# Performance work log

Measured on AMD Instinct MI355X. Metric: run time of the kernel, lower is better.

Reference implementation:

```python
import jax, jax.numpy as jnp
import numpy as np

N_OSC = 256
BATCH = 1024
DT = 0.1
STEPS = 10


def setup_inputs() -> dict:
    key = jax.random.key(0)
    k_theta, k_K, k_omega = jax.random.split(key, 3)
    theta_init = jax.random.normal(k_theta, (BATCH, N_OSC), dtype=jnp.float32)
    K0 = jax.random.normal(k_K, (N_OSC, N_OSC), dtype=jnp.float32) * 0.1
    K = (K0 + K0.T) / 2  # symmetric coupling matrix, as in torch init
    omega = jax.random.normal(k_omega, (N_OSC,), dtype=jnp.float32) * 0.1
    K_global = jnp.float32(0.5)
    return {"theta_init": theta_init, "K": K, "omega": omega, "K_global": K_global}


def reference(theta_init, K, omega, K_global):
    n = K.shape[0]

    def step(theta, _):
        # diff[b, i, j] = theta[b, j] - theta[b, i]
        diff = theta[..., None, :] - theta[..., :, None]
        coupling_sum = jnp.sum(K * jnp.sin(diff), axis=-1)  # (batch, n)
        dtheta = omega + (K_global / n) * coupling_sum
        theta_new = theta + DT * dtheta
        # wrap to (-pi, pi]
        theta_new = jnp.arctan2(jnp.sin(theta_new), jnp.cos(theta_new))
        return theta_new, None

    theta, _ = jax.lax.scan(step, theta_init, None, length=STEPS)
    cos_mean = jnp.cos(theta).mean(axis=-1)
    sin_mean = jnp.sin(theta).mean(axis=-1)
    coherence = jnp.sqrt(cos_mean ** 2 + sin_mean ** 2)
    return theta, coherence
```

## Files before the change

kernel.cpp:

```cpp
#include <hip/hip_runtime.h>
#include <math.h>


typedef __attribute__((ext_vector_type(4))) float f32x4;

constexpr int N       = 256;
constexpr int RB      = 16;
constexpr int STEPS   = 10;
constexpr int WAVES   = 8;
constexpr int THREADS = WAVES * 64;
constexpr float DT    = 0.1f;
constexpr float TWO_PI     = 6.28318530717958648f;
constexpr float INV_TWO_PI = 0.15915494309189535f;

__global__ __launch_bounds__(THREADS, 2)
void kuramoto_fp8(const float* __restrict__ theta0,
                  const float* __restrict__ Kmat,
                  const float* __restrict__ omega,
                  const float* __restrict__ kglob,
                  float* __restrict__ theta_out,
                  float* __restrict__ coh_out)
{
    __shared__ __align__(16) unsigned char SC[2][RB][512];
    __shared__ float redS[RB][WAVES], redC[RB][WAVES];

    const int tid  = threadIdx.x;
    const int wv   = tid >> 6;
    const int lane = tid & 63;
    const int q    = lane >> 4;
    const int l15  = lane & 15;
    const int b0   = blockIdx.x * RB;

    const float kgn = kglob[0] * (1.0f / 256.0f);

    long kf[2][8];
#pragma unroll
    for (int t = 0; t < 2; ++t) {
        const int i = 32 * wv + 16 * t + l15;
        const float* kr = Kmat + (size_t)i * N + 8 * q;
#pragma unroll
        for (int c = 0; c < 8; ++c) {
            float4 lo = *(const float4*)(kr + 32 * c);
            float4 hi = *(const float4*)(kr + 32 * c + 4);
            int w0 = __builtin_amdgcn_cvt_pk_fp8_f32(lo.x, lo.y, 0, false);
            w0     = __builtin_amdgcn_cvt_pk_fp8_f32(lo.z, lo.w, w0, true);
            int w1 = __builtin_amdgcn_cvt_pk_fp8_f32(hi.x, hi.y, 0, false);
            w1     = __builtin_amdgcn_cvt_pk_fp8_f32(hi.z, hi.w, w1, true);
            kf[t][c] = (long)(unsigned)w0 | ((long)w1 << 32);
        }
    }

    float thv[2][4], om[2][4];
#pragma unroll
    for (int t = 0; t < 2; ++t)
#pragma unroll
        for (int r = 0; r < 4; ++r) {
            const int i = 32 * wv + 16 * t + 4 * q + r;
            om[t][r]  = omega[i];
            thv[t][r] = theta0[(size_t)(b0 + l15) * N + i];
        }

    float sv[2][4], cv[2][4];

    for (int s = 0; s < STEPS; ++s) {
        const int buf = s & 1;
#pragma unroll
        for (int t = 0; t < 2; ++t) {
#pragma unroll
            for (int r = 0; r < 4; ++r)
                __sincosf(thv[t][r], &sv[t][r], &cv[t][r]);
            int spk = __builtin_amdgcn_cvt_pk_fp8_f32(sv[t][0], sv[t][1], 0, false);
            spk     = __builtin_amdgcn_cvt_pk_fp8_f32(sv[t][2], sv[t][3], spk, true);
            int cpk = __builtin_amdgcn_cvt_pk_fp8_f32(cv[t][0], cv[t][1], 0, false);
            cpk     = __builtin_amdgcn_cvt_pk_fp8_f32(cv[t][2], cv[t][3], cpk, true);
            const int g = 8 * wv + 4 * t + q;
            const int u = (g >> 1) ^ l15;
            int2 val; val.x = spk; val.y = cpk;
            *(int2*)&SC[buf][l15][16 * u + 8 * (g & 1)] = val;
        }
        __syncthreads();

        f32x4 aS[2], aC[2];
#pragma unroll
        for (int t = 0; t < 2; ++t) {
            aS[t] = (f32x4){0.f, 0.f, 0.f, 0.f};
            aC[t] = (f32x4){0.f, 0.f, 0.f, 0.f};
        }
#pragma unroll
        for (int c = 0; c < 8; ++c) {
            const int uu = (4 * c + q) ^ l15;
            int4 vvv = *(const int4*)&SC[buf][l15][16 * uu];
            long Bs = (long)(unsigned)vvv.x | ((long)vvv.z << 32);
            long Bc = (long)(unsigned)vvv.y | ((long)vvv.w << 32);
#pragma unroll
            for (int t = 0; t < 2; ++t) {
                aS[t] = __builtin_amdgcn_mfma_f32_16x16x32_fp8_fp8(kf[t][c], Bs, aS[t], 0, 0, 0);
                aC[t] = __builtin_amdgcn_mfma_f32_16x16x32_fp8_fp8(kf[t][c], Bc, aC[t], 0, 0, 0);
            }
        }

#pragma unroll
        for (int t = 0; t < 2; ++t)
#pragma unroll
            for (int r = 0; r < 4; ++r) {
                float coup = cv[t][r] * aS[t][r] - sv[t][r] * aC[t][r];
                thv[t][r] = fmaf(DT, fmaf(kgn, coup, om[t][r]), thv[t][r]);
            }
    }

    float ps = 0.f, pc = 0.f;
#pragma unroll
    for (int t = 0; t < 2; ++t)
#pragma unroll
        for (int r = 0; r < 4; ++r) {
            float th = thv[t][r];
            float s0, c0;
            __sincosf(th, &s0, &c0);
            float w = fmaf(-TWO_PI, rintf(th * INV_TWO_PI), th);
            theta_out[(size_t)(b0 + l15) * N + 32 * wv + 16 * t + 4 * q + r] = w;
            ps += s0; pc += c0;
        }
    ps += __shfl_xor(ps, 16, 64);  pc += __shfl_xor(pc, 16, 64);
    ps += __shfl_xor(ps, 32, 64);  pc += __shfl_xor(pc, 32, 64);
    if (q == 0) { redS[l15][wv] = ps; redC[l15][wv] = pc; }
    __syncthreads();
    if (tid < RB) {
        float S = 0.f, C = 0.f;
#pragma unroll
        for (int k = 0; k < WAVES; ++k) { S += redS[tid][k]; C += redC[tid][k]; }
        float sm = S * (1.0f / 256.0f);
        float cm = C * (1.0f / 256.0f);
        coh_out[b0 + tid] = sqrtf(sm * sm + cm * cm);
    }
}

extern "C" void kernel_launch(void* const* d_in, const int* in_sizes, int n_in,
                              void* d_out, int out_size, void* d_ws, size_t ws_size,
                              hipStream_t stream) {
    const float* theta0 = (const float*)d_in[0];
    const float* Kmat   = (const float*)d_in[1];
    const float* omega  = (const float*)d_in[2];
    const float* kglob  = (const float*)d_in[3];

    float* theta_out = (float*)d_out;
    float* coh_out   = theta_out + 1024 * N;

    kuramoto_fp8<<<dim3(1024 / RB), dim3(THREADS), 0, stream>>>(
        theta0, Kmat, omega, kglob, theta_out, coh_out);
}
```

Baseline: 75.19 us.

## Prepack K to fp8 in a separate kernel and update sin/cos via angle-addition polynomials

A small pre-kernel converts K to fp8 in MFMA fragment order once, stored in workspace, so the 64 main blocks no longer each load and convert the full K matrix. The per-step sincos is replaced by a rotation using low-order Taylor sin/cos of the small increment d, removing transcendental calls from the loop. Theta and omega loads and output stores are vectorized to float4, and the final sincos is dropped in favour of the carried sin/cos. This adds a second kernel launch and accumulates polynomial and rotation error over the steps, which can drift from the exact sin/cos of theta.

Result: faster. 70.89 us (-5.7%).

```diff
diff --git a/kernel.cpp b/kernel.cpp
--- a/kernel.cpp
+++ b/kernel.cpp
@@ -3,6 +3,7 @@
 
 
 typedef __attribute__((ext_vector_type(4))) float f32x4;
+typedef __attribute__((ext_vector_type(2))) long long2_t;
 
 constexpr int N       = 256;
 constexpr int RB      = 16;
@@ -13,15 +14,34 @@
 constexpr float TWO_PI     = 6.28318530717958648f;
 constexpr float INV_TWO_PI = 0.15915494309189535f;
 
+__global__ __launch_bounds__(512)
+void pack_k(const float* __restrict__ Kmat, unsigned char* __restrict__ kf8)
+{
+    const int id   = blockIdx.x * blockDim.x + threadIdx.x;
+    const int T    = id >> 9;
+    const int c    = (id >> 6) & 7;
+    const int lane = id & 63;
+    const int q    = lane >> 4, l15 = lane & 15;
+    const float* src = Kmat + (size_t)(16 * T + l15) * N + 32 * c + 8 * q;
+    float4 lo = *(const float4*)src;
+    float4 hi = *(const float4*)(src + 4);
+    int w0 = __builtin_amdgcn_cvt_pk_fp8_f32(lo.x, lo.y, 0, false);
+    w0     = __builtin_amdgcn_cvt_pk_fp8_f32(lo.z, lo.w, w0, true);
+    int w1 = __builtin_amdgcn_cvt_pk_fp8_f32(hi.x, hi.y, 0, false);
+    w1     = __builtin_amdgcn_cvt_pk_fp8_f32(hi.z, hi.w, w1, true);
+    int2 out; out.x = w0; out.y = w1;
+    *(int2*)(kf8 + (size_t)id * 8) = out;
+}
+
 __global__ __launch_bounds__(THREADS, 2)
-void kuramoto_fp8(const float* __restrict__ theta0,
-                  const float* __restrict__ Kmat,
-                  const float* __restrict__ omega,
-                  const float* __restrict__ kglob,
-                  float* __restrict__ theta_out,
-                  float* __restrict__ coh_out)
+void kuramoto_r6(const float* __restrict__ theta0,
+                 const unsigned char* __restrict__ kf8,
+                 const float* __restrict__ omega,
+                 const float* __restrict__ kglob,
+                 float* __restrict__ theta_out,
+                 float* __restrict__ coh_out)
 {
-    __shared__ __align__(16) unsigned char SC[2][RB][512];
+    __shared__ __align__(16) unsigned char SC[2][RB * 512];
     __shared__ float redS[RB][WAVES], redC[RB][WAVES];
 
     const int tid  = threadIdx.x;
@@ -36,90 +56,83 @@
     long kf[2][8];
 #pragma unroll
     for (int t = 0; t < 2; ++t) {
-        const int i = 32 * wv + 16 * t + l15;
-        const float* kr = Kmat + (size_t)i * N + 8 * q;
+        const unsigned char* base = kf8 + (size_t)((2 * wv + t) * 512 + lane) * 8;
 #pragma unroll
-        for (int c = 0; c < 8; ++c) {
-            float4 lo = *(const float4*)(kr + 32 * c);
-            float4 hi = *(const float4*)(kr + 32 * c + 4);
-            int w0 = __builtin_amdgcn_cvt_pk_fp8_f32(lo.x, lo.y, 0, false);
-            w0     = __builtin_amdgcn_cvt_pk_fp8_f32(lo.z, lo.w, w0, true);
-            int w1 = __builtin_amdgcn_cvt_pk_fp8_f32(hi.x, hi.y, 0, false);
-            w1     = __builtin_amdgcn_cvt_pk_fp8_f32(hi.z, hi.w, w1, true);
-            kf[t][c] = (long)(unsigned)w0 | ((long)w1 << 32);
-        }
+        for (int c = 0; c < 8; ++c)
+            kf[t][c] = *(const long*)(base + (size_t)c * 512);
     }
 
-    float thv[2][4], om[2][4];
+    float th[8], om[8], sn[8], cs[8];
 #pragma unroll
-    for (int t = 0; t < 2; ++t)
+    for (int t = 0; t < 2; ++t) {
+        const int ob = 32 * wv + 16 * t + 4 * q;
+        float4 t4 = *(const float4*)(theta0 + (size_t)(b0 + l15) * N + ob);
+        float4 o4 = *(const float4*)(omega + ob);
+        th[4*t+0] = t4.x; th[4*t+1] = t4.y; th[4*t+2] = t4.z; th[4*t+3] = t4.w;
+        om[4*t+0] = o4.x; om[4*t+1] = o4.y; om[4*t+2] = o4.z; om[4*t+3] = o4.w;
+    }
 #pragma unroll
-        for (int r = 0; r < 4; ++r) {
-            const int i = 32 * wv + 16 * t + 4 * q + r;
-            om[t][r]  = omega[i];
-            thv[t][r] = theta0[(size_t)(b0 + l15) * N + i];
-        }
+    for (int k = 0; k < 8; ++k)
+        __sincosf(th[k], &sn[k], &cs[k]);
 
-    float sv[2][4], cv[2][4];
+    const int so = 4 * (q & 1);
+    const int g0 = 4 * wv + (q >> 1);
 
     for (int s = 0; s < STEPS; ++s) {
-        const int buf = s & 1;
+        unsigned char* rowp = &SC[s & 1][l15 * 512];
 #pragma unroll
         for (int t = 0; t < 2; ++t) {
-#pragma unroll
-            for (int r = 0; r < 4; ++r)
-                __sincosf(thv[t][r], &sv[t][r], &cv[t][r]);
-            int spk = __builtin_amdgcn_cvt_pk_fp8_f32(sv[t][0], sv[t][1], 0, false);
-            spk     = __builtin_amdgcn_cvt_pk_fp8_f32(sv[t][2], sv[t][3], spk, true);
-            int cpk = __builtin_amdgcn_cvt_pk_fp8_f32(cv[t][0], cv[t][1], 0, false);
-            cpk     = __builtin_amdgcn_cvt_pk_fp8_f32(cv[t][2], cv[t][3], cpk, true);
-            const int g = 8 * wv + 4 * t + q;
-            const int u = (g >> 1) ^ l15;
-            int2 val; val.x = spk; val.y = cpk;
-            *(int2*)&SC[buf][l15][16 * u + 8 * (g & 1)] = val;
+            int spk = __builtin_amdgcn_cvt_pk_fp8_f32(sn[4*t+0], sn[4*t+1], 0, false);
+            spk     = __builtin_amdgcn_cvt_pk_fp8_f32(sn[4*t+2], sn[4*t+3], spk, true);
+            int cpk = __builtin_amdgcn_cvt_pk_fp8_f32(cs[4*t+0], cs[4*t+1], 0, false);
+            cpk     = __builtin_amdgcn_cvt_pk_fp8_f32(cs[4*t+2], cs[4*t+3], cpk, true);
+            const int base = (((g0 + 2 * t) ^ l15) << 4);
+            *(int*)(rowp + base + so)     = spk;
+            *(int*)(rowp + base + 8 + so) = cpk;
         }
         __syncthreads();
 
         f32x4 aS[2], aC[2];
-#pragma unroll
-        for (int t = 0; t < 2; ++t) {
-            aS[t] = (f32x4){0.f, 0.f, 0.f, 0.f};
-            aC[t] = (f32x4){0.f, 0.f, 0.f, 0.f};
-        }
+        aS[0] = (f32x4){0.f,0.f,0.f,0.f}; aS[1] = (f32x4){0.f,0.f,0.f,0.f};
+        aC[0] = (f32x4){0.f,0.f,0.f,0.f}; aC[1] = (f32x4){0.f,0.f,0.f,0.f};
 #pragma unroll
         for (int c = 0; c < 8; ++c) {
-            const int uu = (4 * c + q) ^ l15;
-            int4 vvv = *(const int4*)&SC[buf][l15][16 * uu];
-            long Bs = (long)(unsigned)vvv.x | ((long)vvv.z << 32);
-            long Bc = (long)(unsigned)vvv.y | ((long)vvv.w << 32);
-#pragma unroll
-            for (int t = 0; t < 2; ++t) {
-                aS[t] = __builtin_amdgcn_mfma_f32_16x16x32_fp8_fp8(kf[t][c], Bs, aS[t], 0, 0, 0);
-                aC[t] = __builtin_amdgcn_mfma_f32_16x16x32_fp8_fp8(kf[t][c], Bc, aC[t], 0, 0, 0);
-            }
+            long2_t v = *(const long2_t*)(rowp + ((((4 * c + q) ^ l15)) << 4));
+            aS[0] = __builtin_amdgcn_mfma_f32_16x16x32_fp8_fp8(kf[0][c], v.x, aS[0], 0, 0, 0);
+            aC[0] = __builtin_amdgcn_mfma_f32_16x16x32_fp8_fp8(kf[0][c], v.y, aC[0], 0, 0, 0);
+            aS[1] = __builtin_amdgcn_mfma_f32_16x16x32_fp8_fp8(kf[1][c], v.x, aS[1], 0, 0, 0);
+            aC[1] = __builtin_amdgcn_mfma_f32_16x16x32_fp8_fp8(kf[1][c], v.y, aC[1], 0, 0, 0);
         }
 
 #pragma unroll
         for (int t = 0; t < 2; ++t)
 #pragma unroll
             for (int r = 0; r < 4; ++r) {
-                float coup = cv[t][r] * aS[t][r] - sv[t][r] * aC[t][r];
-                thv[t][r] = fmaf(DT, fmaf(kgn, coup, om[t][r]), thv[t][r]);
+                const int k = 4 * t + r;
+                float coup = cs[k] * aS[t][r] - sn[k] * aC[t][r];
+                float d  = DT * fmaf(kgn, coup, om[k]);
+                float d2 = d * d;
+                float sd = d * fmaf(d2, -1.0f / 6.0f, 1.0f);
+                float cd = fmaf(d2, fmaf(d2, 1.0f / 24.0f, -0.5f), 1.0f);
+                float s2 = fmaf(sn[k], cd,  cs[k] * sd);
+                float c2 = fmaf(cs[k], cd, -sn[k] * sd);
+                sn[k] = s2; cs[k] = c2; th[k] += d;
             }
     }
 
     float ps = 0.f, pc = 0.f;
 #pragma unroll
-    for (int t = 0; t < 2; ++t)
+    for (int t = 0; t < 2; ++t) {
+        const int ob = 32 * wv + 16 * t + 4 * q;
+        float4 outv;
+        outv.x = fmaf(-TWO_PI, rintf(th[4*t+0] * INV_TWO_PI), th[4*t+0]);
+        outv.y = fmaf(-TWO_PI, rintf(th[4*t+1] * INV_TWO_PI), th[4*t+1]);
+        outv.z = fmaf(-TWO_PI, rintf(th[4*t+2] * INV_TWO_PI), th[4*t+2]);
+        outv.w = fmaf(-TWO_PI, rintf(th[4*t+3] * INV_TWO_PI), th[4*t+3]);
+        *(float4*)(theta_out + (size_t)(b0 + l15) * N + ob) = outv;
 #pragma unroll
-        for (int r = 0; r < 4; ++r) {
-            float th = thv[t][r];
-            float s0, c0;
-            __sincosf(th, &s0, &c0);
-            float w = fmaf(-TWO_PI, rintf(th * INV_TWO_PI), th);
-            theta_out[(size_t)(b0 + l15) * N + 32 * wv + 16 * t + 4 * q + r] = w;
-            ps += s0; pc += c0;
-        }
+        for (int r = 0; r < 4; ++r) { ps += sn[4*t+r]; pc += cs[4*t+r]; }
+    }
     ps += __shfl_xor(ps, 16, 64);  pc += __shfl_xor(pc, 16, 64);
     ps += __shfl_xor(ps, 32, 64);  pc += __shfl_xor(pc, 32, 64);
     if (q == 0) { redS[l15][wv] = ps; redC[l15][wv] = pc; }
@@ -142,9 +155,12 @@
     const float* omega  = (const float*)d_in[2];
     const float* kglob  = (const float*)d_in[3];
 
+    unsigned char* kf8 = (unsigned char*)d_ws;
+
     float* theta_out = (float*)d_out;
     float* coh_out   = theta_out + 1024 * N;
 
-    kuramoto_fp8<<<dim3(1024 / RB), dim3(THREADS), 0, stream>>>(
-        theta0, Kmat, omega, kglob, theta_out, coh_out);
+    pack_k<<<dim3(16), dim3(512), 0, stream>>>(Kmat, kf8);
+    kuramoto_r6<<<dim3(1024 / RB), dim3(THREADS), 0, stream>>>(
+        theta0, kf8, omega, kglob, theta_out, coh_out);
 }
```
